# Kernel optimization log

Measured on AMD Instinct MI355X. Metric: run time of the kernel, lower is better.

The kernel has to match this reference:

```python
import jax, jax.numpy as jnp
import numpy as np

N, N_BINS = 100000, 512
BATCH, K = 8192, 16


def setup_inputs() -> dict:
    key = jax.random.key(0)
    k1, k2, k3 = jax.random.split(key, 3)
    outputs = jax.random.uniform(k1, (N, N_BINS), dtype=jnp.float32)
    # y holds (float-encoded) neighbor indices; trunc(y) must index rows of outputs
    y = jax.random.randint(k2, (BATCH, K), 0, N).astype(jnp.float32)
    weights = jax.random.uniform(k3, (BATCH,), dtype=jnp.float32)
    return {"outputs": outputs, "y": y, "weights": weights}


def reference(outputs, y, weights):
    n, n_bins = outputs.shape
    batch_size, k = y.shape
    nns = jnp.trunc(y).astype(jnp.int32)  # (B, k) indices into outputs rows

    # Torch builds add[a,b,c] = outputs[nns[c,a], b] + outputs[c, b] with shape
    # (k, n_bins, batch) then maxes over bins. Equivalent, batch-major layout:
    o_nn = outputs[nns]  # (B, k, n_bins) gather
    add = jnp.max(o_nn + outputs[:batch_size, None, :], axis=-1)  # (B, k)

    booster_weights = jnp.clip((2.0 - jnp.mean(add, axis=1)) / 2.0, 0.5)  # (B,)
    add_mean = jnp.mean(add * weights[:, None])
    diff = jnp.square(2.0 - add_mean)

    target_b = n / n_bins
    b_col = jnp.sum(outputs[:batch_size], axis=0)  # (n_bins,)
    b = jnp.max(b_col) - jnp.min(b_col)

    cost = b / target_b + diff
    return (cost, diff, b / target_b, booster_weights)
```

## Files before the change

### kernel.cpp

```cpp
#include <hip/hip_runtime.h>

#define NBINS 512
#define BDIM 256

__global__ __launch_bounds__(BDIM) void gather_kernel(
        const float* __restrict__ outputs,
        const float* __restrict__ y,
        float* __restrict__ add,
        int K) {
    const int b    = blockIdx.x;
    const int w    = threadIdx.x >> 6;
    const int lane = threadIdx.x & 63;

    const float4* bp = (const float4*)(outputs + (size_t)b * NBINS);
    const float4  b0 = bp[lane * 2];
    const float4  b1 = bp[lane * 2 + 1];

    const int kbase = w * 4;
    int nn[4];
    #pragma unroll
    for (int j = 0; j < 4; ++j)
        nn[j] = (int)y[b * K + kbase + j];

    float4 g0[4], g1[4];
    #pragma unroll
    for (int j = 0; j < 4; ++j) {
        const float4* gp = (const float4*)(outputs + (size_t)nn[j] * NBINS);
        g0[j] = gp[lane * 2];
        g1[j] = gp[lane * 2 + 1];
    }

    float m[4];
    #pragma unroll
    for (int j = 0; j < 4; ++j) {
        m[j] = fmaxf(fmaxf(fmaxf(g0[j].x + b0.x, g0[j].y + b0.y),
                           fmaxf(g0[j].z + b0.z, g0[j].w + b0.w)),
                     fmaxf(fmaxf(g1[j].x + b1.x, g1[j].y + b1.y),
                           fmaxf(g1[j].z + b1.z, g1[j].w + b1.w)));
    }

    #pragma unroll
    for (int off = 32; off > 0; off >>= 1) {
        #pragma unroll
        for (int j = 0; j < 4; ++j)
            m[j] = fmaxf(m[j], __shfl_down(m[j], off, 64));
    }

    if (lane == 0) {
        float4 v = make_float4(m[0], m[1], m[2], m[3]);
        *((float4*)(add + (size_t)b * K + kbase)) = v;
    }
}

__global__ __launch_bounds__(NBINS) void colsum_kernel(
        const float* __restrict__ outputs,
        float* __restrict__ part,
        int rows_per_block) {
    const int t = threadIdx.x;
    const size_t r0 = (size_t)blockIdx.x * rows_per_block;
    float local = 0.0f;
    for (int r = 0; r < rows_per_block; ++r)
        local += outputs[(r0 + r) * NBINS + t];
    part[(size_t)blockIdx.x * NBINS + t] = local;
}

__global__ __launch_bounds__(BDIM) void booster_kernel(
        const float* __restrict__ add,
        const float* __restrict__ weights,
        float* __restrict__ out,
        float* __restrict__ wpartial,
        int K) {
    __shared__ float sred[BDIM];
    const int t = threadIdx.x;
    const int b = blockIdx.x * BDIM + t;

    const float4* ap = (const float4*)(add + (size_t)b * K);
    float4 a0 = ap[0], a1 = ap[1], a2 = ap[2], a3 = ap[3];
    float sum = ((a0.x + a0.y) + (a0.z + a0.w))
              + ((a1.x + a1.y) + (a1.z + a1.w))
              + ((a2.x + a2.y) + (a2.z + a2.w))
              + ((a3.x + a3.y) + (a3.z + a3.w));

    float booster = fmaxf(0.5f, (2.0f - sum * (1.0f / 16.0f)) * 0.5f);
    out[3 + b] = booster;

    sred[t] = weights[b] * sum;
    __syncthreads();
    for (int s = BDIM / 2; s > 0; s >>= 1) {
        if (t < s) sred[t] += sred[t + s];
        __syncthreads();
    }
    if (t == 0) wpartial[blockIdx.x] = sred[0];
}

__global__ __launch_bounds__(NBINS) void final_kernel(
        const float* __restrict__ part,
        const float* __restrict__ wpartial,
        float* __restrict__ out,
        int npart, int nw, float inv_count, float inv_target) {
    __shared__ float smax[NBINS];
    __shared__ float smin[NBINS];
    const int t = threadIdx.x;
    float v = 0.0f;
    for (int j = 0; j < npart; ++j)
        v += part[(size_t)j * NBINS + t];
    smax[t] = v;
    smin[t] = v;
    __syncthreads();
    for (int s = NBINS / 2; s > 0; s >>= 1) {
        if (t < s) {
            smax[t] = fmaxf(smax[t], smax[t + s]);
            smin[t] = fminf(smin[t], smin[t + s]);
        }
        __syncthreads();
    }
    if (t == 0) {
        float acc = 0.0f;
        for (int i = 0; i < nw; ++i) acc += wpartial[i];
        float add_mean = acc * inv_count;
        float d = 2.0f - add_mean;
        float diff = d * d;
        float bn = (smax[0] - smin[0]) * inv_target;
        out[0] = bn + diff;
        out[1] = diff;
        out[2] = bn;
    }
}

extern "C" void kernel_launch(void* const* d_in, const int* in_sizes, int n_in,
                              void* d_out, int out_size, void* d_ws, size_t ws_size,
                              hipStream_t stream) {
    const float* outputs = (const float*)d_in[0];
    const float* y       = (const float*)d_in[1];
    const float* weights = (const float*)d_in[2];
    float* out = (float*)d_out;

    const int B = in_sizes[2];
    const int K = in_sizes[1] / B;
    const int N = in_sizes[0] / NBINS;

    const int COL_BLOCKS = 256;
    const int rows_per_block = B / COL_BLOCKS;
    const int BOOST_BLOCKS = B / BDIM;

    float* ws      = (float*)d_ws;
    float* add     = ws;
    float* colpart = add + (size_t)B * K;
    float* wpart   = colpart + (size_t)COL_BLOCKS * NBINS;

    gather_kernel<<<B, BDIM, 0, stream>>>(outputs, y, add, K);
    colsum_kernel<<<COL_BLOCKS, NBINS, 0, stream>>>(outputs, colpart, rows_per_block);
    booster_kernel<<<BOOST_BLOCKS, BDIM, 0, stream>>>(add, weights, out, wpart, K);
    final_kernel<<<1, NBINS, 0, stream>>>(colpart, wpart, out,
                                          COL_BLOCKS, BOOST_BLOCKS,
                                          1.0f / (float)(B * K),
                                          (float)NBINS / (float)N);
}
```

Measured before the change: 350.1 us.

## Fuse booster computation into gather kernel and coalesce gather loads

Moves the per-row booster weight and weighted-sum computation into the gather kernel through a small shared-memory reduction, so the separate booster kernel and the intermediate add buffer are removed. The final kernel now does a parallel reduction over the per-row weighted sums. Gather loads change from each lane reading two adjacent float4s to lane-strided float4 accesses across two halves of the row, which gives more coalesced wave accesses. This costs an extra block-wide barrier in the gather kernel and a larger reduction in the single-block final kernel.

Result: no change. 348.7 us (-0.4%).

```diff
diff --git a/kernel.cpp b/kernel.cpp
--- a/kernel.cpp
+++ b/kernel.cpp
@@ -6,15 +6,19 @@
 __global__ __launch_bounds__(BDIM) void gather_kernel(
         const float* __restrict__ outputs,
         const float* __restrict__ y,
-        float* __restrict__ add,
+        const float* __restrict__ weights,
+        float* __restrict__ out,
+        float* __restrict__ wpart,
         int K) {
+    __shared__ float s_add[16];
+
     const int b    = blockIdx.x;
     const int w    = threadIdx.x >> 6;
     const int lane = threadIdx.x & 63;
 
     const float4* bp = (const float4*)(outputs + (size_t)b * NBINS);
-    const float4  b0 = bp[lane * 2];
-    const float4  b1 = bp[lane * 2 + 1];
+    const float4  b0 = bp[lane];
+    const float4  b1 = bp[64 + lane];
 
     const int kbase = w * 4;
     int nn[4];
@@ -26,8 +30,8 @@
     #pragma unroll
     for (int j = 0; j < 4; ++j) {
         const float4* gp = (const float4*)(outputs + (size_t)nn[j] * NBINS);
-        g0[j] = gp[lane * 2];
-        g1[j] = gp[lane * 2 + 1];
+        g0[j] = gp[lane];
+        g1[j] = gp[64 + lane];
     }
 
     float m[4];
@@ -47,8 +51,19 @@
     }
 
     if (lane == 0) {
-        float4 v = make_float4(m[0], m[1], m[2], m[3]);
-        *((float4*)(add + (size_t)b * K + kbase)) = v;
+        s_add[kbase + 0] = m[0];
+        s_add[kbase + 1] = m[1];
+        s_add[kbase + 2] = m[2];
+        s_add[kbase + 3] = m[3];
+    }
+    __syncthreads();
+
+    if (threadIdx.x == 0) {
+        float sum = 0.0f;
+        #pragma unroll
+        for (int i = 0; i < 16; ++i) sum += s_add[i];
+        out[3 + b] = fmaxf(0.5f, (2.0f - sum * (1.0f / 16.0f)) * 0.5f);
+        wpart[b] = weights[b] * sum;
     }
 }
 
@@ -64,60 +79,38 @@
     part[(size_t)blockIdx.x * NBINS + t] = local;
 }
 
-__global__ __launch_bounds__(BDIM) void booster_kernel(
-        const float* __restrict__ add,
-        const float* __restrict__ weights,
-        float* __restrict__ out,
-        float* __restrict__ wpartial,
-        int K) {
-    __shared__ float sred[BDIM];
-    const int t = threadIdx.x;
-    const int b = blockIdx.x * BDIM + t;
-
-    const float4* ap = (const float4*)(add + (size_t)b * K);
-    float4 a0 = ap[0], a1 = ap[1], a2 = ap[2], a3 = ap[3];
-    float sum = ((a0.x + a0.y) + (a0.z + a0.w))
-              + ((a1.x + a1.y) + (a1.z + a1.w))
-              + ((a2.x + a2.y) + (a2.z + a2.w))
-              + ((a3.x + a3.y) + (a3.z + a3.w));
-
-    float booster = fmaxf(0.5f, (2.0f - sum * (1.0f / 16.0f)) * 0.5f);
-    out[3 + b] = booster;
-
-    sred[t] = weights[b] * sum;
-    __syncthreads();
-    for (int s = BDIM / 2; s > 0; s >>= 1) {
-        if (t < s) sred[t] += sred[t + s];
-        __syncthreads();
-    }
-    if (t == 0) wpartial[blockIdx.x] = sred[0];
-}
-
 __global__ __launch_bounds__(NBINS) void final_kernel(
         const float* __restrict__ part,
-        const float* __restrict__ wpartial,
+        const float* __restrict__ wpart,
         float* __restrict__ out,
-        int npart, int nw, float inv_count, float inv_target) {
+        int npart, int B, float inv_count, float inv_target) {
     __shared__ float smax[NBINS];
     __shared__ float smin[NBINS];
+    __shared__ float ssum[NBINS];
     const int t = threadIdx.x;
+
     float v = 0.0f;
     for (int j = 0; j < npart; ++j)
         v += part[(size_t)j * NBINS + t];
     smax[t] = v;
     smin[t] = v;
+
+    float ws = 0.0f;
+    for (int i = t; i < B; i += NBINS)
+        ws += wpart[i];
+    ssum[t] = ws;
     __syncthreads();
+
     for (int s = NBINS / 2; s > 0; s >>= 1) {
         if (t < s) {
             smax[t] = fmaxf(smax[t], smax[t + s]);
             smin[t] = fminf(smin[t], smin[t + s]);
+            ssum[t] += ssum[t + s];
         }
         __syncthreads();
     }
     if (t == 0) {
-        float acc = 0.0f;
-        for (int i = 0; i < nw; ++i) acc += wpartial[i];
-        float add_mean = acc * inv_count;
+        float add_mean = ssum[0] * inv_count;
         float d = 2.0f - add_mean;
         float diff = d * d;
         float bn = (smax[0] - smin[0]) * inv_target;
@@ -141,18 +134,15 @@
 
     const int COL_BLOCKS = 256;
     const int rows_per_block = B / COL_BLOCKS;
-    const int BOOST_BLOCKS = B / BDIM;
 
     float* ws      = (float*)d_ws;
-    float* add     = ws;
-    float* colpart = add + (size_t)B * K;
-    float* wpart   = colpart + (size_t)COL_BLOCKS * NBINS;
+    float* wpart   = ws;
+    float* colpart = wpart + B;
 
-    gather_kernel<<<B, BDIM, 0, stream>>>(outputs, y, add, K);
+    gather_kernel<<<B, BDIM, 0, stream>>>(outputs, y, weights, out, wpart, K);
     colsum_kernel<<<COL_BLOCKS, NBINS, 0, stream>>>(outputs, colpart, rows_per_block);
-    booster_kernel<<<BOOST_BLOCKS, BDIM, 0, stream>>>(add, weights, out, wpart, K);
     final_kernel<<<1, NBINS, 0, stream>>>(colpart, wpart, out,
-                                          COL_BLOCKS, BOOST_BLOCKS,
+                                          COL_BLOCKS, B,
                                           1.0f / (float)(B * K),
                                           (float)NBINS / (float)N);
 }
```
